# Optimization experiments

Measured on AMD Instinct MI355X. Metric: run time of the kernel, lower is better.

The kernel has to match this reference:

```python
import jax, jax.numpy as jnp
import numpy as np

DIM = 384
HEADS = 6
NEG = -1e9  # masked-score fill; equivalent to gathering only kept K/V rows


def setup_inputs() -> dict:
    key = jax.random.key(0)
    ks = jax.random.split(key, 9)
    B, N, C = 1, 4098, DIM
    x = jax.random.normal(ks[0], (B, N, C), dtype=jnp.float32)
    pos = jax.random.normal(ks[1], (B, N + 1, C), dtype=jnp.float32)
    # float mask in [0,1); >=0.5 means 'foreground / keep as key', <0.5 pooled into back token
    mask = jax.random.uniform(ks[2], (B, 1, N - 2), dtype=jnp.float32)
    mask_block = jnp.ones((N + 1,), dtype=jnp.float32)  # positions 0, N-1, N always kept
    Wq = jax.random.normal(ks[3], (C, C), dtype=jnp.float32) * 0.02
    Wk = jax.random.normal(ks[4], (C, C), dtype=jnp.float32) * 0.02
    Wv = jax.random.normal(ks[5], (C, C), dtype=jnp.float32) * 0.02
    Wp = jax.random.normal(ks[6], (C, C), dtype=jnp.float32) * 0.02
    bp = jnp.zeros((C,), dtype=jnp.float32)
    return {"x": x, "pos": pos, "mask": mask, "mask_block": mask_block,
            "Wq": Wq, "Wk": Wk, "Wv": Wv, "Wp": Wp, "bp": bp}


def reference(x, pos, mask, mask_block, Wq, Wk, Wv, Wp, bp):
    B, N, C = x.shape
    H = HEADS
    D = C // H
    scale = D ** -0.5
    eps = 1e-10

    # back token: average of background (mask < 0.5) interior tokens
    reverse = jnp.where(mask < 0.5, 1.0, 0.0)                      # (B,1,N-2)
    pooled = jnp.einsum('bon,bnc->boc', reverse, x[:, 1:N - 1])    # (B,1,C)
    back_tokens = pooled / (reverse.sum(axis=2, keepdims=True) + eps)

    kv_x = jnp.concatenate([x, back_tokens], axis=1)               # (B,N+1,C)
    q_x = x + pos[:, :N]
    k_x = kv_x + pos

    q = (q_x @ Wq.T).reshape(B, N, H, D).transpose(0, 2, 1, 3)       # (B,H,N,D)
    k = (k_x @ Wk.T).reshape(B, N + 1, H, D).transpose(0, 2, 1, 3)   # (B,H,N+1,D)
    v = (kv_x @ Wv.T).reshape(B, N + 1, H, D).transpose(0, 2, 1, 3)  # (B,H,N+1,D)

    # key-selection mask: original gathers rows with mask_block >= 0.5;
    # masked softmax over all N+1 keys is mathematically identical.
    mb = mask_block.at[1:N - 1].set(mask[0, 0])
    keep = mb >= 0.5                                               # (N+1,)

    scores = jnp.einsum('bhqd,bhkd->bhqk', q, k) * scale
    scores = jnp.where(keep[None, None, None, :], scores, NEG)
    attn = jax.nn.softmax(scores, axis=-1)
    out = jnp.einsum('bhqk,bhkd->bhqd', attn, v)
    out = out.transpose(0, 2, 1, 3).reshape(B, N, C)
    return out @ Wp.T + bp
```

## Files before the change

### kernel.cpp

```cpp
#include <hip/hip_runtime.h>
#include <math.h>

#define N_TOK 4098
#define NK_TOK 4099
#define C_DIM 384
#define NKPAD 4160
#define NSLICE 6

typedef short  bh8 __attribute__((ext_vector_type(8)));
typedef float  f32x4 __attribute__((ext_vector_type(4)));
typedef unsigned short ushort;
typedef ushort u4 __attribute__((ext_vector_type(4)));
typedef ushort u8 __attribute__((ext_vector_type(8)));

static __device__ __forceinline__ ushort f2bf(float f) {
  unsigned int u = __float_as_uint(f);
  u = (u + 0x7FFF + ((u >> 16) & 1)) >> 16;
  return (ushort)u;
}
static __device__ __forceinline__ float bf2f(ushort s) {
  return __uint_as_float(((unsigned int)s) << 16);
}

__global__ __launch_bounds__(384) void pool_kernel(
    const float* __restrict__ x, const float* __restrict__ mask,
    float* __restrict__ pooled_part, float* __restrict__ cnt_part) {
  const int b = blockIdx.x, t = threadIdx.x;
  const int r0 = b * 32;
  float acc = 0.f;
  int lc = 0;
  for (int r = r0; r < r0 + 32; ++r)
    if (mask[r] < 0.5f) { acc += x[(size_t)(r + 1) * C_DIM + t]; ++lc; }
  pooled_part[b * C_DIM + t] = acc;
  if (t == 0) cnt_part[b] = (float)lc;
}

__global__ __launch_bounds__(256) void prep_kernel(
    const float* __restrict__ x, const float* __restrict__ pos,
    const float* __restrict__ pooled_part, const float* __restrict__ cnt_part,
    const float* __restrict__ Wq, const float* __restrict__ Wk,
    const float* __restrict__ Wv, const float* __restrict__ Wp,
    const float* __restrict__ mask, const float* __restrict__ mask_block,
    ushort* __restrict__ Aq, ushort* __restrict__ Ak, ushort* __restrict__ Av,
    ushort* __restrict__ Wb, int* __restrict__ nk, int* __restrict__ inv) {
  const int b = blockIdx.x, t = threadIdx.x;
  if (b < 260) {
    __shared__ float sback[C_DIM];
    if (b == 256) {
      float cs = 0.f;
      for (int i = (t & 63); i < 128; i += 64) cs += cnt_part[i];
#pragma unroll
      for (int d = 1; d < 64; d <<= 1) cs += __shfl_xor(cs, d);
      const float ic = 1.f / (cs + 1e-10f);
      for (int c = t; c < C_DIM; c += 256) {
        float s = 0.f;
        for (int p = 0; p < 128; ++p) s += pooled_part[p * C_DIM + c];
        sback[c] = s * ic;
      }
      __syncthreads();
    }
    const int r0 = b * 16;
#pragma unroll
    for (int i = 0; i < 6; ++i) {
      const int idx = i * 1024 + t * 4;
      const int row = r0 + idx / C_DIM, col = idx % C_DIM;
      if (row >= NK_TOK) continue;
      const float4 pv = *(const float4*)&pos[(size_t)row * C_DIM + col];
      float4 xv;
      if (row == NK_TOK - 1)
        xv = make_float4(sback[col], sback[col + 1], sback[col + 2], sback[col + 3]);
      else
        xv = *(const float4*)&x[(size_t)row * C_DIM + col];
      if (row < N_TOK) {
        u4 q4 = {f2bf((xv.x + pv.x) * 0.125f), f2bf((xv.y + pv.y) * 0.125f),
                 f2bf((xv.z + pv.z) * 0.125f), f2bf((xv.w + pv.w) * 0.125f)};
        *(u4*)&Aq[(size_t)row * C_DIM + col] = q4;
      }
      u4 k4 = {f2bf(xv.x + pv.x), f2bf(xv.y + pv.y),
               f2bf(xv.z + pv.z), f2bf(xv.w + pv.w)};
      *(u4*)&Ak[(size_t)row * C_DIM + col] = k4;
      u4 v4 = {f2bf(xv.x), f2bf(xv.y), f2bf(xv.z), f2bf(xv.w)};
      *(u4*)&Av[(size_t)row * C_DIM + col] = v4;
    }
  } else if (b < 292) {
    const int wi = b - 260;
    const float* src = (wi < 8) ? Wq : (wi < 16) ? Wk : (wi < 24) ? Wv : Wp;
    const int base = (wi >> 3) * 147456 + (wi & 7) * 18432;
#pragma unroll 2
    for (int i = 0; i < 18; ++i) {
      const int g = base + i * 1024 + t * 4;
      const float4 v = *(const float4*)&src[(wi & 7) * 18432 + i * 1024 + t * 4];
      u4 o = {f2bf(v.x), f2bf(v.y), f2bf(v.z), f2bf(v.w)};
      *(u4*)&Wb[g] = o;
    }
  } else {
    __shared__ int scnt[256];
    const int j0 = t * 17;
    unsigned int bits = 0;
    int c = 0;
#pragma unroll 1
    for (int u = 0; u < 17; ++u) {
      const int j = j0 + u;
      bool keep = false;
      if (j < NK_TOK)
        keep = (j >= 1 && j <= N_TOK - 2) ? (mask[j - 1] >= 0.5f)
                                          : (mask_block[j] >= 0.5f);
      if (keep) { bits |= 1u << u; ++c; }
    }
    scnt[t] = c;
    __syncthreads();
    for (int d = 1; d < 256; d <<= 1) {
      const int v = scnt[t];
      const int add = (t >= d) ? scnt[t - d] : 0;
      __syncthreads();
      scnt[t] = v + add;
      __syncthreads();
    }
    int base = scnt[t] - c;
    if (t == 255) *nk = scnt[255];
#pragma unroll 1
    for (int u = 0; u < 17; ++u) {
      const int j = j0 + u;
      if (j < NK_TOK) inv[j] = ((bits >> u) & 1) ? base++ : -1;
    }
  }
}

static __device__ __forceinline__ void gemm_core(
    const ushort* __restrict__ A, const ushort* __restrict__ B,
    ushort (* __restrict__ As)[72], ushort (* __restrict__ Bs)[72],
    int t, int w, int quad, int l15, f32x4 acc[4]) {
  const int g = t & 7;
  u8 ra[2], rb[2];
#pragma unroll
  for (int it = 0; it < 2; ++it) {
    const int r = it * 32 + (t >> 3);
    ra[it] = *(const u8*)&A[r * C_DIM + g * 8];
    rb[it] = *(const u8*)&B[r * C_DIM + g * 8];
  }
#pragma unroll 1
  for (int kt = 0; kt < 6; ++kt) {
    __syncthreads();
#pragma unroll
    for (int it = 0; it < 2; ++it) {
      const int r = it * 32 + (t >> 3);
      *(u8*)&As[r][g * 8] = ra[it];
      *(u8*)&Bs[r][g * 8] = rb[it];
    }
    __syncthreads();
    if (kt < 5) {
      const int k0 = (kt + 1) * 64;
#pragma unroll
      for (int it = 0; it < 2; ++it) {
        const int r = it * 32 + (t >> 3);
        ra[it] = *(const u8*)&A[r * C_DIM + k0 + g * 8];
        rb[it] = *(const u8*)&B[r * C_DIM + k0 + g * 8];
      }
    }
    const bh8 b0 = *(const bh8*)&Bs[w * 16 + l15][quad * 8];
    const bh8 b1 = *(const bh8*)&Bs[w * 16 + l15][32 + quad * 8];
#pragma unroll
    for (int mb = 0; mb < 4; ++mb) {
      const bh8 a0 = *(const bh8*)&As[mb * 16 + l15][quad * 8];
      const bh8 a1 = *(const bh8*)&As[mb * 16 + l15][32 + quad * 8];
      acc[mb] = __builtin_amdgcn_mfma_f32_16x16x32_bf16(a0, b0, acc[mb], 0, 0, 0);
      acc[mb] = __builtin_amdgcn_mfma_f32_16x16x32_bf16(a1, b1, acc[mb], 0, 0, 0);
    }
  }
}

__global__ __launch_bounds__(256) void gemm3_kernel(
    const ushort* __restrict__ Aq, const ushort* __restrict__ Ak,
    const ushort* __restrict__ Av, const ushort* __restrict__ Wb,
    const int* __restrict__ inv, ushort* __restrict__ Qh,
    ushort* __restrict__ Kc, ushort* __restrict__ Vt) {
  __shared__ ushort As[64][72], Bs[64][72];
  const int t = threadIdx.x, w = t >> 6, lane = t & 63;
  const int quad = lane >> 4, l15 = lane & 15;
  const int m0 = blockIdx.x * 64;
  const int which = blockIdx.y / 6, h = blockIdx.y % 6;
  const ushort* A = (which == 0 ? Aq : which == 1 ? Ak : Av) + (size_t)m0 * C_DIM;
  const ushort* B = Wb + (size_t)which * 147456 + (size_t)h * 64 * C_DIM;
  f32x4 acc[4];
#pragma unroll
  for (int i = 0; i < 4; ++i) acc[i] = (f32x4){0.f, 0.f, 0.f, 0.f};
  gemm_core(A, B, As, Bs, t, w, quad, l15, acc);
  const int n = w * 16 + l15;
  if (which == 0) {
#pragma unroll
    for (int mb = 0; mb < 4; ++mb)
#pragma unroll
      for (int r = 0; r < 4; ++r) {
        const int m = m0 + mb * 16 + quad * 4 + r;
        if (m < N_TOK) Qh[((size_t)h * N_TOK + m) * 64 + n] = f2bf(acc[mb][r]);
      }
  } else if (which == 1) {
#pragma unroll
    for (int mb = 0; mb < 4; ++mb)
#pragma unroll
      for (int r = 0; r < 4; ++r) {
        const int m = m0 + mb * 16 + quad * 4 + r;
        if (m < NK_TOK) {
          const int slot = inv[m];
          if (slot >= 0) Kc[((size_t)h * NKPAD + slot) * 64 + n] = f2bf(acc[mb][r]);
        }
      }
  } else {
#pragma unroll
    for (int mb = 0; mb < 4; ++mb)
#pragma unroll
      for (int r = 0; r < 4; ++r) {
        const int m = m0 + mb * 16 + quad * 4 + r;
        if (m < NK_TOK) {
          const int slot = inv[m];
          if (slot >= 0) Vt[((size_t)h * 64 + n) * NKPAD + slot] = f2bf(acc[mb][r]);
        }
      }
  }
}

__global__ __launch_bounds__(256) void gemm_out_kernel(
    const ushort* __restrict__ Am, const ushort* __restrict__ Wpb,
    const float* __restrict__ bp, float* __restrict__ out) {
  __shared__ ushort As[64][72], Bs[64][72];
  const int t = threadIdx.x, w = t >> 6, lane = t & 63;
  const int quad = lane >> 4, l15 = lane & 15;
  const int m0 = blockIdx.x * 64;
  const int h = blockIdx.y;
  f32x4 acc[4];
#pragma unroll
  for (int i = 0; i < 4; ++i) acc[i] = (f32x4){0.f, 0.f, 0.f, 0.f};
  gemm_core(Am + (size_t)m0 * C_DIM, Wpb + (size_t)h * 64 * C_DIM,
            As, Bs, t, w, quad, l15, acc);
  const int n = w * 16 + l15;
  const float bb = bp[h * 64 + n];
#pragma unroll
  for (int mb = 0; mb < 4; ++mb)
#pragma unroll
    for (int r = 0; r < 4; ++r) {
      const int m = m0 + mb * 16 + quad * 4 + r;
      if (m < N_TOK) out[(size_t)m * C_DIM + h * 64 + n] = acc[mb][r] + bb;
    }
}

__global__ __launch_bounds__(256) void attn_kernel(
    const ushort* __restrict__ Qh, const ushort* __restrict__ Kc,
    const ushort* __restrict__ Vt, const int* __restrict__ nkp,
    ushort* __restrict__ Opart, float* __restrict__ Lpart) {
  __shared__ ushort Ks[64][72];
  __shared__ ushort Vs[64][72];
  __shared__ ushort Ps[4][32][72];
  const int t = threadIdx.x, w = t >> 6, lane = t & 63;
  const int quad = lane >> 4, l15 = lane & 15;
  const int h = blockIdx.y, slice = blockIdx.z;
  const int q0 = blockIdx.x * 128;
  const int nk = *nkp, nchunk = (nk + 63) >> 6;
  const int g = t & 7;

  bh8 qf[2][2];
#pragma unroll
  for (int qa = 0; qa < 2; ++qa) {
    int qr = q0 + w * 32 + qa * 16 + l15;
    if (qr > N_TOK - 1) qr = N_TOK - 1;
    const ushort* qp = Qh + ((size_t)h * N_TOK + qr) * 64 + quad * 8;
    qf[qa][0] = *(const bh8*)qp;
    qf[qa][1] = *(const bh8*)(qp + 32);
  }
  f32x4 oacc[2][4];
#pragma unroll
  for (int qa = 0; qa < 2; ++qa)
#pragma unroll
    for (int i = 0; i < 4; ++i) oacc[qa][i] = (f32x4){0.f, 0.f, 0.f, 0.f};
  float l_r[2] = {0.f, 0.f};

  const ushort* kb = Kc + (size_t)h * NKPAD * 64;
  const ushort* vb = Vt + (size_t)h * 64 * NKPAD;

  u8 rk[2], rv[2];
  if (slice < nchunk) {
#pragma unroll
    for (int it = 0; it < 2; ++it) {
      const int r = it * 32 + (t >> 3);
      rk[it] = *(const u8*)&kb[(size_t)(slice * 64 + r) * 64 + g * 8];
      rv[it] = *(const u8*)&vb[(size_t)r * NKPAD + slice * 64 + g * 8];
    }
  }
#pragma unroll 1
  for (int kc = slice; kc < nchunk; kc += NSLICE) {
    __syncthreads();
#pragma unroll
    for (int it = 0; it < 2; ++it) {
      const int r = it * 32 + (t >> 3);
      *(u8*)&Ks[r][g * 8] = rk[it];
      *(u8*)&Vs[r][g * 8] = rv[it];
    }
    __syncthreads();
    if (kc + NSLICE < nchunk) {
#pragma unroll
      for (int it = 0; it < 2; ++it) {
        const int r = it * 32 + (t >> 3);
        rk[it] = *(const u8*)&kb[(size_t)((kc + NSLICE) * 64 + r) * 64 + g * 8];
        rv[it] = *(const u8*)&vb[(size_t)r * NKPAD + (kc + NSLICE) * 64 + g * 8];
      }
    }
    float csum[2] = {0.f, 0.f};
#pragma unroll
    for (int f = 0; f < 4; ++f) {
      const bh8 a0 = *(const bh8*)&Ks[f * 16 + l15][quad * 8];
      const bh8 a1 = *(const bh8*)&Ks[f * 16 + l15][32 + quad * 8];
      f32x4 s4[2];
#pragma unroll
      for (int qa = 0; qa < 2; ++qa) {
        s4[qa] = (f32x4){0.f, 0.f, 0.f, 0.f};
        s4[qa] = __builtin_amdgcn_mfma_f32_16x16x32_bf16(a0, qf[qa][0], s4[qa], 0, 0, 0);
        s4[qa] = __builtin_amdgcn_mfma_f32_16x16x32_bf16(a1, qf[qa][1], s4[qa], 0, 0, 0);
      }
      const int keyb = kc * 64 + f * 16 + quad * 4;
#pragma unroll
      for (int qa = 0; qa < 2; ++qa) {
        u4 pv;
#pragma unroll
        for (int r = 0; r < 4; ++r) {
          const float p = (keyb + r < nk) ? __expf(s4[qa][r]) : 0.f;
          csum[qa] += p;
          pv[r] = f2bf(p);
        }
        *(u4*)&Ps[w][qa * 16 + l15][f * 16 + quad * 4] = pv;
      }
    }
#pragma unroll
    for (int qa = 0; qa < 2; ++qa) {
      csum[qa] += __shfl_xor(csum[qa], 16);
      csum[qa] += __shfl_xor(csum[qa], 32);
      l_r[qa] += csum[qa];
    }

    bh8 pa[2][2];
#pragma unroll
    for (int qa = 0; qa < 2; ++qa) {
      pa[qa][0] = *(const bh8*)&Ps[w][qa * 16 + l15][quad * 8];
      pa[qa][1] = *(const bh8*)&Ps[w][qa * 16 + l15][32 + quad * 8];
    }
#pragma unroll
    for (int db = 0; db < 4; ++db) {
      const bh8 b0 = *(const bh8*)&Vs[db * 16 + l15][quad * 8];
      const bh8 b1 = *(const bh8*)&Vs[db * 16 + l15][32 + quad * 8];
#pragma unroll
      for (int qa = 0; qa < 2; ++qa) {
        oacc[qa][db] = __builtin_amdgcn_mfma_f32_16x16x32_bf16(pa[qa][0], b0, oacc[qa][db], 0, 0, 0);
        oacc[qa][db] = __builtin_amdgcn_mfma_f32_16x16x32_bf16(pa[qa][1], b1, oacc[qa][db], 0, 0, 0);
      }
    }
  }

  const int sh = slice * 6 + h;
#pragma unroll
  for (int qa = 0; qa < 2; ++qa) {
    const int qg = q0 + w * 32 + qa * 16;
#pragma unroll
    for (int db = 0; db < 4; ++db)
#pragma unroll
      for (int r = 0; r < 4; ++r) {
        const int q = qg + quad * 4 + r;
        if (q < N_TOK)
          Opart[((size_t)sh * NKPAD + q) * 64 + db * 16 + l15] = f2bf(oacc[qa][db][r]);
      }
    if (quad == 0) {
      const int q = qg + l15;
      if (q < N_TOK) Lpart[sh * NKPAD + q] = l_r[qa];
    }
  }
}

__global__ __launch_bounds__(256) void merge_kernel(const ushort* __restrict__ Opart,
                                                    const float* __restrict__ Lpart,
                                                    ushort* __restrict__ Am) {
  const int idx = blockIdx.x * 256 + threadIdx.x;
  if (idx >= N_TOK * 48) return;
  const int q = idx / 48, c = (idx % 48) * 8;
  const int h = c >> 6, d = c & 63;
  float l = 0.f;
#pragma unroll
  for (int s = 0; s < NSLICE; ++s) l += Lpart[(s * 6 + h) * NKPAD + q];
  const float inv = 1.f / l;
  float o[8] = {0.f, 0.f, 0.f, 0.f, 0.f, 0.f, 0.f, 0.f};
#pragma unroll
  for (int s = 0; s < NSLICE; ++s) {
    const u8 v = *(const u8*)&Opart[((size_t)(s * 6 + h) * NKPAD + q) * 64 + d];
#pragma unroll
    for (int j = 0; j < 8; ++j) o[j] += bf2f(v[j]);
  }
  u8 r;
#pragma unroll
  for (int j = 0; j < 8; ++j) r[j] = f2bf(o[j] * inv);
  *(u8*)&Am[(size_t)q * C_DIM + c] = r;
}

extern "C" void kernel_launch(void* const* d_in, const int* in_sizes, int n_in,
                              void* d_out, int out_size, void* d_ws, size_t ws_size,
                              hipStream_t stream) {
  const float* x          = (const float*)d_in[0];
  const float* pos        = (const float*)d_in[1];
  const float* mask       = (const float*)d_in[2];
  const float* mask_block = (const float*)d_in[3];
  const float* Wq         = (const float*)d_in[4];
  const float* Wk         = (const float*)d_in[5];
  const float* Wv         = (const float*)d_in[6];
  const float* Wp         = (const float*)d_in[7];
  const float* bp         = (const float*)d_in[8];
  float* out = (float*)d_out;
  char* wsb = (char*)d_ws;

  float*  pooled_part = (float*)wsb;
  float*  cnt_part    = (float*)(wsb + 196608);
  int*    nk          = (int*)(wsb + 197120);
  int*    inv         = (int*)(wsb + 197632);
  ushort* Aq          = (ushort*)(wsb + 215296);
  ushort* Ak          = (ushort*)(wsb + 3410176);
  ushort* Av          = (ushort*)(wsb + 6605056);
  ushort* Wb          = (ushort*)(wsb + 9799936);
  ushort* Qh          = (ushort*)(wsb + 10979584);
  ushort* Kc          = (ushort*)(wsb + 14126848);
  ushort* Vt          = (ushort*)(wsb + 17321728);
  ushort* Am          = (ushort*)(wsb + 24011008);
  ushort* Op          = (ushort*)(wsb + 27205888);
  float*  Lp          = (float*)(wsb + 46375168);

  pool_kernel<<<dim3(128), dim3(384), 0, stream>>>(x, mask, pooled_part, cnt_part);
  prep_kernel<<<dim3(293), dim3(256), 0, stream>>>(x, pos, pooled_part, cnt_part,
                                                   Wq, Wk, Wv, Wp, mask, mask_block,
                                                   Aq, Ak, Av, Wb, nk, inv);
  gemm3_kernel<<<dim3(65, 18), 256, 0, stream>>>(Aq, Ak, Av, Wb, inv, Qh, Kc, Vt);
  attn_kernel<<<dim3(33, 6, NSLICE), 256, 0, stream>>>(Qh, Kc, Vt, nk, Op, Lp);
  merge_kernel<<<dim3(769), 256, 0, stream>>>(Op, Lp, Am);
  gemm_out_kernel<<<dim3(65, 6), 256, 0, stream>>>(Am, Wb + 3 * 147456, bp, out);
}
```

Measured before the change: 155.3 us.

## Load K/V and weight fragments directly from global memory, dropping LDS staging

```diff
diff --git a/kernel.cpp b/kernel.cpp
--- a/kernel.cpp
+++ b/kernel.cpp
@@ -126,39 +126,31 @@
   }
 }
 
-static __device__ __forceinline__ void gemm_core(
+static __device__ __forceinline__ void gemm_coreA(
     const ushort* __restrict__ A, const ushort* __restrict__ B,
-    ushort (* __restrict__ As)[72], ushort (* __restrict__ Bs)[72],
+    ushort (* __restrict__ As)[72],
     int t, int w, int quad, int l15, f32x4 acc[4]) {
   const int g = t & 7;
-  u8 ra[2], rb[2];
-#pragma unroll
-  for (int it = 0; it < 2; ++it) {
-    const int r = it * 32 + (t >> 3);
-    ra[it] = *(const u8*)&A[r * C_DIM + g * 8];
-    rb[it] = *(const u8*)&B[r * C_DIM + g * 8];
-  }
+  const int r = t >> 3;
+  u8 ra[2];
+#pragma unroll
+  for (int it = 0; it < 2; ++it)
+    ra[it] = *(const u8*)&A[(it * 32 + r) * C_DIM + g * 8];
+  const ushort* bp = B + (size_t)(w * 16 + l15) * C_DIM + quad * 8;
 #pragma unroll 1
   for (int kt = 0; kt < 6; ++kt) {
+    const bh8 b0 = *(const bh8*)(bp + kt * 64);
+    const bh8 b1 = *(const bh8*)(bp + kt * 64 + 32);
     __syncthreads();
 #pragma unroll
-    for (int it = 0; it < 2; ++it) {
-      const int r = it * 32 + (t >> 3);
-      *(u8*)&As[r][g * 8] = ra[it];
-      *(u8*)&Bs[r][g * 8] = rb[it];
-    }
+    for (int it = 0; it < 2; ++it)
+      *(u8*)&As[it * 32 + r][g * 8] = ra[it];
     __syncthreads();
     if (kt < 5) {
-      const int k0 = (kt + 1) * 64;
-#pragma unroll
-      for (int it = 0; it < 2; ++it) {
-        const int r = it * 32 + (t >> 3);
-        ra[it] = *(const u8*)&A[r * C_DIM + k0 + g * 8];
-        rb[it] = *(const u8*)&B[r * C_DIM + k0 + g * 8];
-      }
-    }
-    const bh8 b0 = *(const bh8*)&Bs[w * 16 + l15][quad * 8];
-    const bh8 b1 = *(const bh8*)&Bs[w * 16 + l15][32 + quad * 8];
+#pragma unroll
+      for (int it = 0; it < 2; ++it)
+        ra[it] = *(const u8*)&A[(it * 32 + r) * C_DIM + (kt + 1) * 64 + g * 8];
+    }
 #pragma unroll
     for (int mb = 0; mb < 4; ++mb) {
       const bh8 a0 = *(const bh8*)&As[mb * 16 + l15][quad * 8];
@@ -174,7 +166,7 @@
     const ushort* __restrict__ Av, const ushort* __restrict__ Wb,
     const int* __restrict__ inv, ushort* __restrict__ Qh,
     ushort* __restrict__ Kc, ushort* __restrict__ Vt) {
-  __shared__ ushort As[64][72], Bs[64][72];
+  __shared__ ushort As[64][72];
   const int t = threadIdx.x, w = t >> 6, lane = t & 63;
   const int quad = lane >> 4, l15 = lane & 15;
   const int m0 = blockIdx.x * 64;
@@ -184,7 +176,7 @@
   f32x4 acc[4];
 #pragma unroll
   for (int i = 0; i < 4; ++i) acc[i] = (f32x4){0.f, 0.f, 0.f, 0.f};
-  gemm_core(A, B, As, Bs, t, w, quad, l15, acc);
+  gemm_coreA(A, B, As, t, w, quad, l15, acc);
   const int n = w * 16 + l15;
   if (which == 0) {
 #pragma unroll
@@ -222,7 +214,7 @@
 __global__ __launch_bounds__(256) void gemm_out_kernel(
     const ushort* __restrict__ Am, const ushort* __restrict__ Wpb,
     const float* __restrict__ bp, float* __restrict__ out) {
-  __shared__ ushort As[64][72], Bs[64][72];
+  __shared__ ushort As[64][72];
   const int t = threadIdx.x, w = t >> 6, lane = t & 63;
   const int quad = lane >> 4, l15 = lane & 15;
   const int m0 = blockIdx.x * 64;
@@ -230,8 +222,8 @@
   f32x4 acc[4];
 #pragma unroll
   for (int i = 0; i < 4; ++i) acc[i] = (f32x4){0.f, 0.f, 0.f, 0.f};
-  gemm_core(Am + (size_t)m0 * C_DIM, Wpb + (size_t)h * 64 * C_DIM,
-            As, Bs, t, w, quad, l15, acc);
+  gemm_coreA(Am + (size_t)m0 * C_DIM, Wpb + (size_t)h * 64 * C_DIM,
+             As, t, w, quad, l15, acc);
   const int n = w * 16 + l15;
   const float bb = bp[h * 64 + n];
 #pragma unroll
@@ -247,15 +239,12 @@
     const ushort* __restrict__ Qh, const ushort* __restrict__ Kc,
     const ushort* __restrict__ Vt, const int* __restrict__ nkp,
     ushort* __restrict__ Opart, float* __restrict__ Lpart) {
-  __shared__ ushort Ks[64][72];
-  __shared__ ushort Vs[64][72];
   __shared__ ushort Ps[4][32][72];
   const int t = threadIdx.x, w = t >> 6, lane = t & 63;
   const int quad = lane >> 4, l15 = lane & 15;
   const int h = blockIdx.y, slice = blockIdx.z;
   const int q0 = blockIdx.x * 128;
   const int nk = *nkp, nchunk = (nk + 63) >> 6;
-  const int g = t & 7;
 
   bh8 qf[2][2];
 #pragma unroll
@@ -276,38 +265,14 @@
   const ushort* kb = Kc + (size_t)h * NKPAD * 64;
   const ushort* vb = Vt + (size_t)h * 64 * NKPAD;
 
-  u8 rk[2], rv[2];
-  if (slice < nchunk) {
-#pragma unroll
-    for (int it = 0; it < 2; ++it) {
-      const int r = it * 32 + (t >> 3);
-      rk[it] = *(const u8*)&kb[(size_t)(slice * 64 + r) * 64 + g * 8];
-      rv[it] = *(const u8*)&vb[(size_t)r * NKPAD + slice * 64 + g * 8];
-    }
-  }
 #pragma unroll 1
   for (int kc = slice; kc < nchunk; kc += NSLICE) {
-    __syncthreads();
-#pragma unroll
-    for (int it = 0; it < 2; ++it) {
-      const int r = it * 32 + (t >> 3);
-      *(u8*)&Ks[r][g * 8] = rk[it];
-      *(u8*)&Vs[r][g * 8] = rv[it];
-    }
-    __syncthreads();
-    if (kc + NSLICE < nchunk) {
-#pragma unroll
-      for (int it = 0; it < 2; ++it) {
-        const int r = it * 32 + (t >> 3);
-        rk[it] = *(const u8*)&kb[(size_t)((kc + NSLICE) * 64 + r) * 64 + g * 8];
-        rv[it] = *(const u8*)&vb[(size_t)r * NKPAD + (kc + NSLICE) * 64 + g * 8];
-      }
-    }
+    const ushort* kp0 = kb + ((size_t)kc * 64 + l15) * 64 + quad * 8;
     float csum[2] = {0.f, 0.f};
 #pragma unroll
     for (int f = 0; f < 4; ++f) {
-      const bh8 a0 = *(const bh8*)&Ks[f * 16 + l15][quad * 8];
-      const bh8 a1 = *(const bh8*)&Ks[f * 16 + l15][32 + quad * 8];
+      const bh8 a0 = *(const bh8*)(kp0 + f * 1024);
+      const bh8 a1 = *(const bh8*)(kp0 + f * 1024 + 32);
       f32x4 s4[2];
 #pragma unroll
       for (int qa = 0; qa < 2; ++qa) {
@@ -341,10 +306,11 @@
       pa[qa][0] = *(const bh8*)&Ps[w][qa * 16 + l15][quad * 8];
       pa[qa][1] = *(const bh8*)&Ps[w][qa * 16 + l15][32 + quad * 8];
     }
+    const ushort* vp0 = vb + (size_t)l15 * NKPAD + kc * 64 + quad * 8;
 #pragma unroll
     for (int db = 0; db < 4; ++db) {
-      const bh8 b0 = *(const bh8*)&Vs[db * 16 + l15][quad * 8];
-      const bh8 b1 = *(const bh8*)&Vs[db * 16 + l15][32 + quad * 8];
+      const bh8 b0 = *(const bh8*)(vp0 + (size_t)db * 16 * NKPAD);
+      const bh8 b1 = *(const bh8*)(vp0 + (size_t)db * 16 * NKPAD + 32);
 #pragma unroll
       for (int qa = 0; qa < 2; ++qa) {
         oacc[qa][db] = __builtin_amdgcn_mfma_f32_16x16x32_bf16(pa[qa][0], b0, oacc[qa][db], 0, 0, 0);
```

Result: slower. 194.1 us (+25.0%).
